# Kernel tuning notes

Hardware: AMD Instinct MI355X
Metric: run time of the kernel (lower is better)

## Reference

```python
import jax, jax.numpy as jnp
import numpy as np

# --- simulation constants (from MPMSimulator.__init__ / builder calls) ---
N_STEPS, N_SUBSTEPS = 20, 30          # 20 frames x 30 substeps = 600 iterations
G = 100                               # grid cells per axis (unit domain)
DX, INV_DX = 0.01, 100.0
DT = 5e-4                             # sim_dt
E, NU = 1.0e5, 0.3
MU = E / (2.0 * (1.0 + NU))
LAM = E * NU / ((1.0 + NU) * (1.0 - 2.0 * NU))
P_VOL = 0.005 ** 3                    # particle spacing 0.005
P_MASS = P_VOL * 3000.0               # density 3000
BOUND = 3                             # sticky boundary thickness (cells)
GRAVITY = np.array([0.0, -9.8, 0.0], np.float32)
_o = np.arange(3)
OFFS = np.stack(np.meshgrid(_o, _o, _o, indexing='ij'), -1).reshape(-1, 3).astype(np.int32)  # (27,3)


def setup_inputs() -> dict:
    key = jax.random.key(0)
    k1, k2 = jax.random.split(key)
    nx, ny, nz, sp = 30, 15, 30, 0.005   # add_mpm_grid dims, jitter=True
    gx = (np.arange(nx) - nx / 2) * sp + 0.5
    gy = np.arange(ny) * sp + 0.2
    gz = (np.arange(nz) - nz / 2) * sp + 0.5
    q = np.stack(np.meshgrid(gx, gy, gz, indexing='ij'), -1).reshape(-1, 3).astype(np.float32)
    jitter = jax.random.uniform(k1, q.shape, jnp.float32, 0.0, 0.5 * sp)
    particle_q = jnp.asarray(q) + jitter
    particle_qd = jnp.zeros_like(particle_q)
    v = jax.random.uniform(k2, (1,), jnp.float32, 0.5e-3, 1.5e-3)  # grid_m_ini value
    return {"v": v, "particle_q": particle_q, "particle_qd": particle_qd}


def _simulate(v, particle_q, particle_qd):
    vscalar = v[0]
    offs = jnp.asarray(OFFS)
    offs_f = offs.astype(jnp.float32)
    grav = jnp.asarray(GRAVITY)
    I3 = jnp.eye(3, dtype=jnp.float32)

    def substep(carry, _):
        x, vel, C, F = carry
        # update deformation gradient, neo-Hookean PK1 stress
        F = jnp.einsum('nij,njk->nik', I3 + DT * C, F)
        J = jnp.linalg.det(F)
        FinvT = jnp.swapaxes(jnp.linalg.inv(F), 1, 2)
        logJ = jnp.log(jnp.maximum(J, 1e-6))
        P = MU * (F - FinvT) + LAM * logJ[:, None, None] * FinvT
        stress = (-DT * P_VOL * 4.0 * INV_DX * INV_DX) * jnp.einsum('nij,nkj->nik', P, F)
        affine = stress + P_MASS * C

        # quadratic B-spline weights over 3x3x3 stencil
        base = jnp.floor(x * INV_DX - 0.5).astype(jnp.int32)          # (N,3)
        fx = x * INV_DX - base.astype(jnp.float32)                    # (N,3)
        w = jnp.stack([0.5 * (1.5 - fx) ** 2,
                       0.75 - (fx - 1.0) ** 2,
                       0.5 * (fx - 0.5) ** 2], 0)                     # (3,N,3)
        weight = (w[offs[:, 0], :, 0] * w[offs[:, 1], :, 1] * w[offs[:, 2], :, 2]).T  # (N,27)
        dpos = (offs_f[None] - fx[:, None, :]) * DX                   # (N,27,3)

        # P2G scatter (gravity folded into momentum, as p2g takes gravity)
        mom = weight[..., None] * (P_MASS * (vel + DT * grav)[:, None, :]
                                   + jnp.einsum('nij,nkj->nki', affine, dpos))  # (N,27,3)
        node = jnp.clip(base[:, None, :] + offs[None], 0, G - 1)
        idx = (node[..., 0] * G + node[..., 1]) * G + node[..., 2]    # (N,27)
        idxf = idx.reshape(-1)
        grid_v = jnp.zeros((G * G * G, 3), jnp.float32).at[idxf].add(mom.reshape(-1, 3))
        grid_m = jnp.zeros((G * G * G,), jnp.float32).at[idxf].add((weight * P_MASS).reshape(-1))

        # grid op: grid mass is initialized to grid_m_ini = v (set_optim_variables)
        gv = grid_v / (grid_m + vscalar)[:, None]
        gv3 = gv.reshape(G, G, G, 3)
        for axis in range(3):  # sticky-ish domain boundary (set_grid_bound)
            sh = [1, 1, 1]; sh[axis] = G
            ii = jnp.arange(G).reshape(sh)
            comp = gv3[..., axis]
            comp = jnp.where((ii < BOUND) & (comp < 0), 0.0, comp)
            comp = jnp.where((ii >= G - BOUND) & (comp > 0), 0.0, comp)
            gv3 = gv3.at[..., axis].set(comp)
        gv = gv3.reshape(-1, 3)

        # G2P gather
        gathered = gv[idx]                                            # (N,27,3)
        new_v = jnp.einsum('nk,nki->ni', weight, gathered)
        new_C = (4.0 * INV_DX * INV_DX) * jnp.einsum('nk,nki,nkj->nij', weight, gathered, dpos)
        return (x + DT * new_v, new_v, new_C, F), grid_m

    substep_ck = jax.checkpoint(substep)

    def frame(carry, _):
        carry, gms = jax.lax.scan(substep_ck, carry, None, length=N_SUBSTEPS)
        # extract_grad_tensor: grid mass of last substep (incl. grid_m_ini offset)
        return carry, gms[-1].reshape(G, G, G) + vscalar

    n = particle_q.shape[0]
    carry0 = (particle_q, particle_qd,
              jnp.zeros((n, 3, 3), jnp.float32),
              jnp.tile(I3, (n, 1, 1)))
    _, grid_m_seq = jax.lax.scan(jax.checkpoint(frame), carry0, None, length=N_STEPS)
    return grid_m_seq  # (N_STEPS, G, G, G)


def reference(v, particle_q, particle_qd):
    return _simulate(v, particle_q, particle_qd)
```

## Files before the change

kernel.cpp:

```cpp
#include <hip/hip_runtime.h>
#include <hip/hip_cooperative_groups.h>

namespace cg = cooperative_groups;

static constexpr int G    = 100;
static constexpr int G3   = G * G * G;
static constexpr int NP   = 13500;
static constexpr int NSUB = 600;
static constexpr int SPF  = 30;
static constexpr int NTHR = 512;
static constexpr int NBLK = 108;
static constexpr int TCIN  = 2048;
static constexpr int TCOUT = 2048;
static constexpr int CH   = (G3 + SPF - 2) / (SPF - 1);

__device__ __forceinline__ int clampi(int v) {
    return v < 0 ? 0 : (v > G - 1 ? G - 1 : v);
}
__device__ __forceinline__ int maxi(int a, int b) { return a > b ? a : b; }
__device__ __forceinline__ int mini(int a, int b) { return a < b ? a : b; }

__device__ __forceinline__ float4 cell_load(const float4* p) {
    const unsigned long long* q = reinterpret_cast<const unsigned long long*>(p);
    unsigned long long a = __hip_atomic_load(&q[0], __ATOMIC_RELAXED, __HIP_MEMORY_SCOPE_AGENT);
    unsigned long long b = __hip_atomic_load(&q[1], __ATOMIC_RELAXED, __HIP_MEMORY_SCOPE_AGENT);
    float4 r;
    r.x = __uint_as_float((unsigned)(a & 0xffffffffu));
    r.y = __uint_as_float((unsigned)(a >> 32));
    r.z = __uint_as_float((unsigned)(b & 0xffffffffu));
    r.w = __uint_as_float((unsigned)(b >> 32));
    return r;
}
__device__ __forceinline__ void cell_zero(float4* p) {
    unsigned long long* q = reinterpret_cast<unsigned long long*>(p);
    __hip_atomic_store(&q[0], 0ull, __ATOMIC_RELAXED, __HIP_MEMORY_SCOPE_AGENT);
    __hip_atomic_store(&q[1], 0ull, __ATOMIC_RELAXED, __HIP_MEMORY_SCOPE_AGENT);
}

__device__ __forceinline__ void gridbar(unsigned* __restrict__ cnt,
                                        unsigned* __restrict__ flag,
                                        unsigned gen) {
    __syncthreads();
    if (threadIdx.x == 0) {
        const unsigned old = __hip_atomic_fetch_add(cnt, 1u, __ATOMIC_RELAXED, __HIP_MEMORY_SCOPE_AGENT);
        if (old == gen * (unsigned)NBLK - 1u) {
            __hip_atomic_store(flag, gen, __ATOMIC_RELEASE, __HIP_MEMORY_SCOPE_AGENT);
        }
    }
    while (__hip_atomic_load(flag, __ATOMIC_RELAXED, __HIP_MEMORY_SCOPE_AGENT) < gen) { }
    asm volatile("" ::: "memory");
}

__launch_bounds__(NTHR)
__global__ void mpm_sim(const float* __restrict__ vscal,
                        const float* __restrict__ q0,
                        const float* __restrict__ qd0,
                        float* __restrict__ out,
                        float* __restrict__ ws,
                        unsigned* __restrict__ barcnt,
                        unsigned* __restrict__ barflag)
{
    const float vs = vscal[0];
    float4* const g4 = reinterpret_cast<float4*>(ws);

    cg::grid_group gg = cg::this_grid();
    const int tid = blockIdx.x * NTHR + threadIdx.x;
    const int nth = NBLK * NTHR;

    const int slot = threadIdx.x >> 2;
    const int sub  = threadIdx.x & 3;
    const bool act = slot < 125;
    int pid = 0;
    if (act) {
        const int b  = blockIdx.x;
        const int bx = b / 18;
        const int by = (b / 6) % 3;
        const int bz = b % 6;
        const int lx = slot / 25;
        const int rem = slot % 25;
        const int ly = rem / 5;
        const int lz = rem % 5;
        const int ix = bx * 5 + lx;
        const int iy = by * 5 + ly;
        const int iz = bz * 5 + lz;
        pid = (ix * 15 + iy) * 30 + iz;
    }

    const float DT      = 5e-4f;
    const float INV_DX  = 100.0f;
    const float DXc     = 0.01f;
    const float MU      = (float)(1.0e5 / (2.0 * (1.0 + 0.3)));
    const float LAM     = (float)(1.0e5 * 0.3 / ((1.0 + 0.3) * (1.0 - 0.6)));
    const float P_MASS  = (float)(0.005 * 0.005 * 0.005 * 3000.0);
    const float KS      = (float)(-5.0e-4 * (0.005 * 0.005 * 0.005) * 4.0 * 100.0 * 100.0);
    const float DTG     = (float)(5.0e-4 * (-9.8));
    const float CSC     = 4.0f * INV_DX * INV_DX;

    __shared__ float4 tileIn[TCIN];
    __shared__ float  tileOut[4 * TCOUT];
    __shared__ int sred[6];

    {
        const float4 z = make_float4(0.f, 0.f, 0.f, 0.f);
        for (int i = tid; i < 3 * G3; i += nth) g4[i] = z;
        if (tid == 0) {
            __hip_atomic_store(barcnt,  0u, __ATOMIC_RELAXED, __HIP_MEMORY_SCOPE_AGENT);
            __hip_atomic_store(barflag, 0u, __ATOMIC_RELAXED, __HIP_MEMORY_SCOPE_AGENT);
        }
    }

    float px = 0.f, py = 0.f, pz = 0.f, vx = 0.f, vy = 0.f, vz = 0.f;
    float C00 = 0.f, C01 = 0.f, C02 = 0.f,
          C10 = 0.f, C11 = 0.f, C12 = 0.f,
          C20 = 0.f, C21 = 0.f, C22 = 0.f;
    float F00 = 1.f, F01 = 0.f, F02 = 0.f,
          F10 = 0.f, F11 = 1.f, F12 = 0.f,
          F20 = 0.f, F21 = 0.f, F22 = 1.f;
    if (act) {
        px = q0[3 * pid + 0]; py = q0[3 * pid + 1]; pz = q0[3 * pid + 2];
        vx = qd0[3 * pid + 0]; vy = qd0[3 * pid + 1]; vz = qd0[3 * pid + 2];
    }

    int pmn0 = 0, pmn1 = 0, pmn2 = 0, pmx0 = -1, pmx1 = -1, pmx2 = -1; bool pvalid = false;
    int zmn0 = 0, zmn1 = 0, zmn2 = 0, zmx0 = -1, zmx1 = -1, zmx2 = -1; bool zvalid = false;

    gg.sync();

    unsigned gen = 0;

    for (int p = 0; p < NSUB; ++p) {
        const int bS = p % 3;
        const int bG = (p + 2) % 3;
        const int bZ = (p + 1) % 3;
        float4*       __restrict__ gS4 = g4 + bS * G3;
        const float4* __restrict__ gG4 = g4 + bG * G3;
        float4*       __restrict__ gZ4 = g4 + bZ * G3;
        const int fc = p % SPF;
        float* const outF = (fc == SPF - 1) ? (out + (p / SPF) * G3) : nullptr;

        const int tmn0 = pvalid ? maxi(pmn0 - 1, 0) : 0;
        const int tmn1 = pvalid ? maxi(pmn1 - 1, 0) : 0;
        const int tmn2 = pvalid ? maxi(pmn2 - 1, 0) : 0;
        const int tD0  = pvalid ? (mini(pmx0 + 1, G - 1) - tmn0 + 1) : 0;
        const int tD1  = pvalid ? (mini(pmx1 + 1, G - 1) - tmn1 + 1) : 0;
        const int tD2  = pvalid ? (mini(pmx2 + 1, G - 1) - tmn2 + 1) : 0;
        const int tvol = pvalid ? tD0 * tD1 * tD2 : 0;
        const bool fast = pvalid && (tvol <= TCOUT);

        if (threadIdx.x == 0) {
            sred[0] = INT_MAX; sred[1] = INT_MAX; sred[2] = INT_MAX;
            sred[3] = INT_MIN; sred[4] = INT_MIN; sred[5] = INT_MIN;
        }
        if (fc < SPF - 1) {
            float* of = out + (p / SPF) * G3;
            const int beg = fc * CH;
            const int end = (beg + CH < G3) ? beg + CH : G3;
            for (int i = beg + tid; i < end; i += nth)
                __hip_atomic_store(&of[i], vs, __ATOMIC_RELAXED, __HIP_MEMORY_SCOPE_AGENT);
        }
        {
            float4* t4 = reinterpret_cast<float4*>(tileOut);
            const float4 z = make_float4(0.f, 0.f, 0.f, 0.f);
            const int zn = fast ? tvol : TCOUT;
            for (int i = threadIdx.x; i < zn; i += NTHR) t4[i] = z;
        }
        if (zvalid) {
            const int zD1 = zmx1 - zmn1 + 1, zD2 = zmx2 - zmn2 + 1;
            const int zvol = (zmx0 - zmn0 + 1) * zD1 * zD2;
            for (int c = threadIdx.x; c < zvol; c += NTHR) {
                const int k = c % zD2;
                const int t = c / zD2;
                const int j = t % zD1;
                const int i = t / zD1;
                cell_zero(&gZ4[((zmn0 + i) * G + (zmn1 + j)) * G + (zmn2 + k)]);
            }
        }
        const int iD1 = pvalid ? (pmx1 - pmn1 + 1) : 0;
        const int iD2 = pvalid ? (pmx2 - pmn2 + 1) : 0;
        const int inVol = pvalid ? (pmx0 - pmn0 + 1) * iD1 * iD2 : 0;
        const bool staged = pvalid && (inVol <= TCIN);
        if (staged) {
            for (int c = threadIdx.x; c < inVol; c += NTHR) {
                const int k = c % iD2;
                const int t = c / iD2;
                const int j = t % iD1;
                const int i = t / iD1;
                const int nx = pmn0 + i, ny = pmn1 + j, nz = pmn2 + k;
                const float4 gq = cell_load(&gG4[(nx * G + ny) * G + nz]);
                const float den = gq.w + vs;
                float gvx = gq.x / den;
                float gvy = gq.y / den;
                float gvz = gq.z / den;
                if (nx < 3       && gvx < 0.f) gvx = 0.f;
                if (nx >= G - 3  && gvx > 0.f) gvx = 0.f;
                if (ny < 3       && gvy < 0.f) gvy = 0.f;
                if (ny >= G - 3  && gvy > 0.f) gvy = 0.f;
                if (nz < 3       && gvz < 0.f) gvz = 0.f;
                if (nz >= G - 3  && gvz > 0.f) gvz = 0.f;
                tileIn[c] = make_float4(gvx, gvy, gvz, 0.f);
            }
        }
        __syncthreads();

        int sb0 = 0, sb1 = 0, sb2 = 0;
        float fx0 = 0.f, fx1 = 0.f, fx2 = 0.f;
        float A00 = 0.f, A01 = 0.f, A02 = 0.f,
              A10 = 0.f, A11 = 0.f, A12 = 0.f,
              A20 = 0.f, A21 = 0.f, A22 = 0.f;
        float mvx = 0.f, mvy = 0.f, mvz = 0.f;

        if (act) {
            if (p > 0) {
                const float xs0 = px * INV_DX, xs1 = py * INV_DX, xs2 = pz * INV_DX;
                const float fb0 = floorf(xs0 - 0.5f), fb1 = floorf(xs1 - 0.5f), fb2 = floorf(xs2 - 0.5f);
                const int b0 = (int)fb0, b1 = (int)fb1, b2 = (int)fb2;
                const float gx0 = xs0 - fb0, gx1 = xs1 - fb1, gx2 = xs2 - fb2;
                float wa[3], wb[3], wc[3];
                wa[0] = 0.5f * (1.5f - gx0) * (1.5f - gx0);
                wa[1] = 0.75f - (gx0 - 1.0f) * (gx0 - 1.0f);
                wa[2] = 0.5f * (gx0 - 0.5f) * (gx0 - 0.5f);
                wb[0] = 0.5f * (1.5f - gx1) * (1.5f - gx1);
                wb[1] = 0.75f - (gx1 - 1.0f) * (gx1 - 1.0f);
                wb[2] = 0.5f * (gx1 - 0.5f) * (gx1 - 0.5f);
                wc[0] = 0.5f * (1.5f - gx2) * (1.5f - gx2);
                wc[1] = 0.75f - (gx2 - 1.0f) * (gx2 - 1.0f);
                wc[2] = 0.5f * (gx2 - 0.5f) * (gx2 - 0.5f);

                float nvx = 0.f, nvy = 0.f, nvz = 0.f;
                float nc00 = 0.f, nc01 = 0.f, nc02 = 0.f,
                      nc10 = 0.f, nc11 = 0.f, nc12 = 0.f,
                      nc20 = 0.f, nc21 = 0.f, nc22 = 0.f;
                #pragma unroll
                for (int t = 0; t < 7; ++t) {
                    const int c = sub + 4 * t;
                    if (c >= 27) break;
                    const int oi = c / 9;
                    const int rem = c - 9 * oi;
                    const int oj = rem / 3;
                    const int ok = rem - 3 * oj;
                    const int nx = clampi(b0 + oi);
                    const int ny = clampi(b1 + oj);
                    const int nz = clampi(b2 + ok);
                    const float dpx = ((float)oi - gx0) * DXc;
                    const float dpy = ((float)oj - gx1) * DXc;
                    const float dpz = ((float)ok - gx2) * DXc;
                    const float w = wa[oi] * wb[oj] * wc[ok];
                    float gvx, gvy, gvz;
                    if (staged) {
                        const float4 gv4 = tileIn[((nx - pmn0) * iD1 + (ny - pmn1)) * iD2 + (nz - pmn2)];
                        gvx = gv4.x; gvy = gv4.y; gvz = gv4.z;
                    } else {
                        const float4 gq = cell_load(&gG4[(nx * G + ny) * G + nz]);
                        const float den = gq.w + vs;
                        gvx = gq.x / den;
                        gvy = gq.y / den;
                        gvz = gq.z / den;
                        if (nx < 3       && gvx < 0.f) gvx = 0.f;
                        if (nx >= G - 3  && gvx > 0.f) gvx = 0.f;
                        if (ny < 3       && gvy < 0.f) gvy = 0.f;
                        if (ny >= G - 3  && gvy > 0.f) gvy = 0.f;
                        if (nz < 3       && gvz < 0.f) gvz = 0.f;
                        if (nz >= G - 3  && gvz > 0.f) gvz = 0.f;
                    }
                    nvx += w * gvx; nvy += w * gvy; nvz += w * gvz;
                    const float wgx = w * gvx, wgy = w * gvy, wgz = w * gvz;
                    nc00 += wgx * dpx; nc01 += wgx * dpy; nc02 += wgx * dpz;
                    nc10 += wgy * dpx; nc11 += wgy * dpy; nc12 += wgy * dpz;
                    nc20 += wgz * dpx; nc21 += wgz * dpy; nc22 += wgz * dpz;
                }
                #define BFLY(v) { v += __shfl_xor(v, 1); v += __shfl_xor(v, 2); }
                BFLY(nvx) BFLY(nvy) BFLY(nvz)
                BFLY(nc00) BFLY(nc01) BFLY(nc02)
                BFLY(nc10) BFLY(nc11) BFLY(nc12)
                BFLY(nc20) BFLY(nc21) BFLY(nc22)
                #undef BFLY
                vx = nvx; vy = nvy; vz = nvz;
                C00 = CSC * nc00; C01 = CSC * nc01; C02 = CSC * nc02;
                C10 = CSC * nc10; C11 = CSC * nc11; C12 = CSC * nc12;
                C20 = CSC * nc20; C21 = CSC * nc21; C22 = CSC * nc22;
                px += DT * vx; py += DT * vy; pz += DT * vz;
            }

            {
                const float t00 = F00 + DT * (C00 * F00 + C01 * F10 + C02 * F20);
                const float t01 = F01 + DT * (C00 * F01 + C01 * F11 + C02 * F21);
                const float t02 = F02 + DT * (C00 * F02 + C01 * F12 + C02 * F22);
                const float t10 = F10 + DT * (C10 * F00 + C11 * F10 + C12 * F20);
                const float t11 = F11 + DT * (C10 * F01 + C11 * F11 + C12 * F21);
                const float t12 = F12 + DT * (C10 * F02 + C11 * F12 + C12 * F22);
                const float t20 = F20 + DT * (C20 * F00 + C21 * F10 + C22 * F20);
                const float t21 = F21 + DT * (C20 * F01 + C21 * F11 + C22 * F21);
                const float t22 = F22 + DT * (C20 * F02 + C21 * F12 + C22 * F22);
                F00 = t00; F01 = t01; F02 = t02;
                F10 = t10; F11 = t11; F12 = t12;
                F20 = t20; F21 = t21; F22 = t22;
            }

            const float c00 = F11 * F22 - F12 * F21;
            const float c01 = F12 * F20 - F10 * F22;
            const float c02 = F10 * F21 - F11 * F20;
            const float det = F00 * c00 + F01 * c01 + F02 * c02;
            const float c10 = F02 * F21 - F01 * F22;
            const float c11 = F00 * F22 - F02 * F20;
            const float c12 = F01 * F20 - F00 * F21;
            const float c20 = F01 * F12 - F02 * F11;
            const float c21 = F02 * F10 - F00 * F12;
            const float c22 = F00 * F11 - F01 * F10;
            const float idet = 1.0f / det;
            const float lj = LAM * logf(fmaxf(det, 1e-6f));
            const float fit00 = c00 * idet, fit01 = c01 * idet, fit02 = c02 * idet;
            const float fit10 = c10 * idet, fit11 = c11 * idet, fit12 = c12 * idet;
            const float fit20 = c20 * idet, fit21 = c21 * idet, fit22 = c22 * idet;
            const float P00 = MU * (F00 - fit00) + lj * fit00;
            const float P01 = MU * (F01 - fit01) + lj * fit01;
            const float P02 = MU * (F02 - fit02) + lj * fit02;
            const float P10 = MU * (F10 - fit10) + lj * fit10;
            const float P11 = MU * (F11 - fit11) + lj * fit11;
            const float P12 = MU * (F12 - fit12) + lj * fit12;
            const float P20 = MU * (F20 - fit20) + lj * fit20;
            const float P21 = MU * (F21 - fit21) + lj * fit21;
            const float P22 = MU * (F22 - fit22) + lj * fit22;
            A00 = KS * (P00 * F00 + P01 * F01 + P02 * F02) + P_MASS * C00;
            A01 = KS * (P00 * F10 + P01 * F11 + P02 * F12) + P_MASS * C01;
            A02 = KS * (P00 * F20 + P01 * F21 + P02 * F22) + P_MASS * C02;
            A10 = KS * (P10 * F00 + P11 * F01 + P12 * F02) + P_MASS * C10;
            A11 = KS * (P10 * F10 + P11 * F11 + P12 * F12) + P_MASS * C11;
            A12 = KS * (P10 * F20 + P11 * F21 + P12 * F22) + P_MASS * C12;
            A20 = KS * (P20 * F00 + P21 * F01 + P22 * F02) + P_MASS * C20;
            A21 = KS * (P20 * F10 + P21 * F11 + P22 * F12) + P_MASS * C21;
            A22 = KS * (P20 * F20 + P21 * F21 + P22 * F22) + P_MASS * C22;

            const float xs0 = px * INV_DX, xs1 = py * INV_DX, xs2 = pz * INV_DX;
            const float fb0 = floorf(xs0 - 0.5f), fb1 = floorf(xs1 - 0.5f), fb2 = floorf(xs2 - 0.5f);
            sb0 = (int)fb0; sb1 = (int)fb1; sb2 = (int)fb2;
            fx0 = xs0 - fb0; fx1 = xs1 - fb1; fx2 = xs2 - fb2;
            mvx = P_MASS * vx;
            mvy = P_MASS * (vy + DTG);
            mvz = P_MASS * vz;

            if (sub == 0) {
                atomicMin(&sred[0], clampi(sb0)); atomicMax(&sred[3], clampi(sb0 + 2));
                atomicMin(&sred[1], clampi(sb1)); atomicMax(&sred[4], clampi(sb1 + 2));
                atomicMin(&sred[2], clampi(sb2)); atomicMax(&sred[5], clampi(sb2 + 2));
            }
        }

        float wa0 = 0.f, wa1 = 0.f, wa2 = 0.f, wb0 = 0.f, wb1 = 0.f, wb2 = 0.f,
              wcc0 = 0.f, wcc1 = 0.f, wcc2 = 0.f;
        if (act) {
            wa0 = 0.5f * (1.5f - fx0) * (1.5f - fx0);
            wa1 = 0.75f - (fx0 - 1.0f) * (fx0 - 1.0f);
            wa2 = 0.5f * (fx0 - 0.5f) * (fx0 - 0.5f);
            wb0 = 0.5f * (1.5f - fx1) * (1.5f - fx1);
            wb1 = 0.75f - (fx1 - 1.0f) * (fx1 - 1.0f);
            wb2 = 0.5f * (fx1 - 0.5f) * (fx1 - 0.5f);
            wcc0 = 0.5f * (1.5f - fx2) * (1.5f - fx2);
            wcc1 = 0.75f - (fx2 - 1.0f) * (fx2 - 1.0f);
            wcc2 = 0.5f * (fx2 - 0.5f) * (fx2 - 0.5f);
        }
        const float WA[3] = { wa0, wa1, wa2 };
        const float WB[3] = { wb0, wb1, wb2 };
        const float WC[3] = { wcc0, wcc1, wcc2 };

        if (fast) {
            if (act) {
                #pragma unroll
                for (int t = 0; t < 7; ++t) {
                    const int c = sub + 4 * t;
                    if (c >= 27) break;
                    const int oi = c / 9;
                    const int rem = c - 9 * oi;
                    const int oj = rem / 3;
                    const int ok = rem - 3 * oj;
                    const int li  = clampi(sb0 + oi) - tmn0;
                    const int lj2 = clampi(sb1 + oj) - tmn1;
                    const int lk  = clampi(sb2 + ok) - tmn2;
                    const float dpx = ((float)oi - fx0) * DXc;
                    const float dpy = ((float)oj - fx1) * DXc;
                    const float dpz = ((float)ok - fx2) * DXc;
                    const float w = WA[oi] * WB[oj] * WC[ok];
                    const int c4 = 4 * ((li * tD1 + lj2) * tD2 + lk);
                    atomicAdd(&tileOut[c4 + 0], w * (mvx + A00 * dpx + A01 * dpy + A02 * dpz));
                    atomicAdd(&tileOut[c4 + 1], w * (mvy + A10 * dpx + A11 * dpy + A12 * dpz));
                    atomicAdd(&tileOut[c4 + 2], w * (mvz + A20 * dpx + A21 * dpy + A22 * dpz));
                    atomicAdd(&tileOut[c4 + 3], w * P_MASS);
                }
            }
            __syncthreads();
            for (int c = threadIdx.x; c < tvol; c += NTHR) {
                const float m = tileOut[4 * c + 3];
                if (m != 0.f) {
                    const int k = c % tD2;
                    const int t = c / tD2;
                    const int j = t % tD1;
                    const int i = t / tD1;
                    const int gidx = ((tmn0 + i) * G + (tmn1 + j)) * G + (tmn2 + k);
                    float* gp = reinterpret_cast<float*>(gS4 + gidx);
                    unsafeAtomicAdd(gp + 0, tileOut[4 * c + 0]);
                    unsafeAtomicAdd(gp + 1, tileOut[4 * c + 1]);
                    unsafeAtomicAdd(gp + 2, tileOut[4 * c + 2]);
                    unsafeAtomicAdd(gp + 3, m);
                    if (outF) unsafeAtomicAdd(&outF[gidx], m);
                }
            }
        } else {
            __syncthreads();
            const int mn0 = sred[0], mn1 = sred[1], mn2 = sred[2];
            const int mx0 = sred[3], mx1 = sred[4], mx2 = sred[5];
            const bool anyAct = (mx0 >= mn0);
            const int D1 = mx1 - mn1 + 1, D2 = mx2 - mn2 + 1;
            const int vol = anyAct ? (mx0 - mn0 + 1) * D1 * D2 : 0;
            const bool useLDS = anyAct && (vol <= TCOUT);
            if (useLDS) {
                if (act) {
                    #pragma unroll
                    for (int t = 0; t < 7; ++t) {
                        const int c = sub + 4 * t;
                        if (c >= 27) break;
                        const int oi = c / 9;
                        const int rem = c - 9 * oi;
                        const int oj = rem / 3;
                        const int ok = rem - 3 * oj;
                        const int li  = clampi(sb0 + oi) - mn0;
                        const int lj2 = clampi(sb1 + oj) - mn1;
                        const int lk  = clampi(sb2 + ok) - mn2;
                        const float dpx = ((float)oi - fx0) * DXc;
                        const float dpy = ((float)oj - fx1) * DXc;
                        const float dpz = ((float)ok - fx2) * DXc;
                        const float w = WA[oi] * WB[oj] * WC[ok];
                        const int c4 = 4 * ((li * D1 + lj2) * D2 + lk);
                        atomicAdd(&tileOut[c4 + 0], w * (mvx + A00 * dpx + A01 * dpy + A02 * dpz));
                        atomicAdd(&tileOut[c4 + 1], w * (mvy + A10 * dpx + A11 * dpy + A12 * dpz));
                        atomicAdd(&tileOut[c4 + 2], w * (mvz + A20 * dpx + A21 * dpy + A22 * dpz));
                        atomicAdd(&tileOut[c4 + 3], w * P_MASS);
                    }
                }
                __syncthreads();
                for (int c = threadIdx.x; c < vol; c += NTHR) {
                    const float m = tileOut[4 * c + 3];
                    if (m != 0.f) {
                        const int k = c % D2;
                        const int t = c / D2;
                        const int j = t % D1;
                        const int i = t / D1;
                        const int gidx = ((mn0 + i) * G + (mn1 + j)) * G + (mn2 + k);
                        float* gp = reinterpret_cast<float*>(gS4 + gidx);
                        unsafeAtomicAdd(gp + 0, tileOut[4 * c + 0]);
                        unsafeAtomicAdd(gp + 1, tileOut[4 * c + 1]);
                        unsafeAtomicAdd(gp + 2, tileOut[4 * c + 2]);
                        unsafeAtomicAdd(gp + 3, m);
                        if (outF) unsafeAtomicAdd(&outF[gidx], m);
                    }
                }
            } else {
                if (anyAct && act) {
                    #pragma unroll
                    for (int t = 0; t < 7; ++t) {
                        const int c = sub + 4 * t;
                        if (c >= 27) break;
                        const int oi = c / 9;
                        const int rem = c - 9 * oi;
                        const int oj = rem / 3;
                        const int ok = rem - 3 * oj;
                        const int nx = clampi(sb0 + oi);
                        const int ny = clampi(sb1 + oj);
                        const int nz = clampi(sb2 + ok);
                        const float dpx = ((float)oi - fx0) * DXc;
                        const float dpy = ((float)oj - fx1) * DXc;
                        const float dpz = ((float)ok - fx2) * DXc;
                        const float w = WA[oi] * WB[oj] * WC[ok];
                        const int gidx = (nx * G + ny) * G + nz;
                        float* gp = reinterpret_cast<float*>(gS4 + gidx);
                        unsafeAtomicAdd(gp + 0, w * (mvx + A00 * dpx + A01 * dpy + A02 * dpz));
                        unsafeAtomicAdd(gp + 1, w * (mvy + A10 * dpx + A11 * dpy + A12 * dpz));
                        unsafeAtomicAdd(gp + 2, w * (mvz + A20 * dpx + A21 * dpy + A22 * dpz));
                        unsafeAtomicAdd(gp + 3, w * P_MASS);
                        if (outF) unsafeAtomicAdd(&outF[gidx], w * P_MASS);
                    }
                }
                __syncthreads();
            }
        }

        zmn0 = pmn0; zmn1 = pmn1; zmn2 = pmn2;
        zmx0 = pmx0; zmx1 = pmx1; zmx2 = pmx2; zvalid = pvalid;
        pmn0 = sred[0]; pmn1 = sred[1]; pmn2 = sred[2];
        pmx0 = sred[3]; pmx1 = sred[4]; pmx2 = sred[5]; pvalid = (pmx0 >= pmn0);

        if (p < NSUB - 1) gridbar(barcnt, barflag, ++gen);
    }
}

extern "C" void kernel_launch(void* const* d_in, const int* in_sizes, int n_in,
                              void* d_out, int out_size, void* d_ws, size_t ws_size,
                              hipStream_t stream) {
    const float* v  = (const float*)d_in[0];
    const float* q  = (const float*)d_in[1];
    const float* qd = (const float*)d_in[2];
    float* out = (float*)d_out;
    float* ws  = (float*)d_ws;
    char* tail = (char*)d_ws + (ws_size & ~(size_t)255);
    unsigned* barcnt  = reinterpret_cast<unsigned*>(tail - 256);
    unsigned* barflag = reinterpret_cast<unsigned*>(tail - 512);
    void* args[] = { (void*)&v, (void*)&q, (void*)&qd, (void*)&out, (void*)&ws,
                     (void*)&barcnt, (void*)&barflag };
    hipLaunchCooperativeKernel(reinterpret_cast<void*>(mpm_sim),
                               dim3(NBLK), dim3(NTHR), args, 0, stream);
}
```

Measured before the change: 17.49 ms.

## Use LDS-only barriers and single-thread global spin in grid barrier

Replaces __syncthreads with a custom barrier that waits only on LDS counters (lgkmcnt) instead of all outstanding memory ops. The grid barrier now has only thread 0 spin on the global flag and broadcast via a shared-memory flag, so the other threads stop polling global memory. Zeroing and output-fill work is moved after the staged input load so global stores can stay in flight across the block barrier. This risks memory-ordering bugs, because the global stores and atomics are no longer drained before barriers.

Measured after the change: 17.28 ms. About the same (-1.2%).

```diff
diff --git a/kernel.cpp b/kernel.cpp
--- a/kernel.cpp
+++ b/kernel.cpp
@@ -1,5 +1,6 @@
 #include <hip/hip_runtime.h>
 #include <hip/hip_cooperative_groups.h>
+#include <climits>
 
 namespace cg = cooperative_groups;
 
@@ -37,18 +38,11 @@
     __hip_atomic_store(&q[1], 0ull, __ATOMIC_RELAXED, __HIP_MEMORY_SCOPE_AGENT);
 }
 
-__device__ __forceinline__ void gridbar(unsigned* __restrict__ cnt,
-                                        unsigned* __restrict__ flag,
-                                        unsigned gen) {
-    __syncthreads();
-    if (threadIdx.x == 0) {
-        const unsigned old = __hip_atomic_fetch_add(cnt, 1u, __ATOMIC_RELAXED, __HIP_MEMORY_SCOPE_AGENT);
-        if (old == gen * (unsigned)NBLK - 1u) {
-            __hip_atomic_store(flag, gen, __ATOMIC_RELEASE, __HIP_MEMORY_SCOPE_AGENT);
-        }
-    }
-    while (__hip_atomic_load(flag, __ATOMIC_RELAXED, __HIP_MEMORY_SCOPE_AGENT) < gen) { }
-    asm volatile("" ::: "memory");
+__device__ __forceinline__ void bar_lds() {
+    __builtin_amdgcn_sched_barrier(0);
+    asm volatile("s_waitcnt lgkmcnt(0)" ::: "memory");
+    __builtin_amdgcn_s_barrier();
+    __builtin_amdgcn_sched_barrier(0);
 }
 
 __launch_bounds__(NTHR)
@@ -99,6 +93,7 @@
     __shared__ float4 tileIn[TCIN];
     __shared__ float  tileOut[4 * TCOUT];
     __shared__ int sred[6];
+    __shared__ unsigned lflag;
 
     {
         const float4 z = make_float4(0.f, 0.f, 0.f, 0.f);
@@ -107,6 +102,7 @@
             __hip_atomic_store(barcnt,  0u, __ATOMIC_RELAXED, __HIP_MEMORY_SCOPE_AGENT);
             __hip_atomic_store(barflag, 0u, __ATOMIC_RELAXED, __HIP_MEMORY_SCOPE_AGENT);
         }
+        if (threadIdx.x == 0) lflag = 0u;
     }
 
     float px = 0.f, py = 0.f, pz = 0.f, vx = 0.f, vy = 0.f, vz = 0.f;
@@ -147,34 +143,6 @@
         const int tvol = pvalid ? tD0 * tD1 * tD2 : 0;
         const bool fast = pvalid && (tvol <= TCOUT);
 
-        if (threadIdx.x == 0) {
-            sred[0] = INT_MAX; sred[1] = INT_MAX; sred[2] = INT_MAX;
-            sred[3] = INT_MIN; sred[4] = INT_MIN; sred[5] = INT_MIN;
-        }
-        if (fc < SPF - 1) {
-            float* of = out + (p / SPF) * G3;
-            const int beg = fc * CH;
-            const int end = (beg + CH < G3) ? beg + CH : G3;
-            for (int i = beg + tid; i < end; i += nth)
-                __hip_atomic_store(&of[i], vs, __ATOMIC_RELAXED, __HIP_MEMORY_SCOPE_AGENT);
-        }
-        {
-            float4* t4 = reinterpret_cast<float4*>(tileOut);
-            const float4 z = make_float4(0.f, 0.f, 0.f, 0.f);
-            const int zn = fast ? tvol : TCOUT;
-            for (int i = threadIdx.x; i < zn; i += NTHR) t4[i] = z;
-        }
-        if (zvalid) {
-            const int zD1 = zmx1 - zmn1 + 1, zD2 = zmx2 - zmn2 + 1;
-            const int zvol = (zmx0 - zmn0 + 1) * zD1 * zD2;
-            for (int c = threadIdx.x; c < zvol; c += NTHR) {
-                const int k = c % zD2;
-                const int t = c / zD2;
-                const int j = t % zD1;
-                const int i = t / zD1;
-                cell_zero(&gZ4[((zmn0 + i) * G + (zmn1 + j)) * G + (zmn2 + k)]);
-            }
-        }
         const int iD1 = pvalid ? (pmx1 - pmn1 + 1) : 0;
         const int iD2 = pvalid ? (pmx2 - pmn2 + 1) : 0;
         const int inVol = pvalid ? (pmx0 - pmn0 + 1) * iD1 * iD2 : 0;
@@ -200,7 +168,35 @@
                 tileIn[c] = make_float4(gvx, gvy, gvz, 0.f);
             }
         }
-        __syncthreads();
+        {
+            float4* t4 = reinterpret_cast<float4*>(tileOut);
+            const float4 z = make_float4(0.f, 0.f, 0.f, 0.f);
+            const int zn = fast ? tvol : TCOUT;
+            for (int i = threadIdx.x; i < zn; i += NTHR) t4[i] = z;
+        }
+        if (zvalid) {
+            const int zD1 = zmx1 - zmn1 + 1, zD2 = zmx2 - zmn2 + 1;
+            const int zvol = (zmx0 - zmn0 + 1) * zD1 * zD2;
+            for (int c = threadIdx.x; c < zvol; c += NTHR) {
+                const int k = c % zD2;
+                const int t = c / zD2;
+                const int j = t % zD1;
+                const int i = t / zD1;
+                cell_zero(&gZ4[((zmn0 + i) * G + (zmn1 + j)) * G + (zmn2 + k)]);
+            }
+        }
+        if (fc < SPF - 1) {
+            float* of = out + (p / SPF) * G3;
+            const int beg = fc * CH;
+            const int end = (beg + CH < G3) ? beg + CH : G3;
+            for (int i = beg + tid; i < end; i += nth)
+                __hip_atomic_store(&of[i], vs, __ATOMIC_RELAXED, __HIP_MEMORY_SCOPE_AGENT);
+        }
+        if (threadIdx.x == 0) {
+            sred[0] = INT_MAX; sred[1] = INT_MAX; sred[2] = INT_MAX;
+            sred[3] = INT_MIN; sred[4] = INT_MIN; sred[5] = INT_MIN;
+        }
+        bar_lds();
 
         int sb0 = 0, sb1 = 0, sb2 = 0;
         float fx0 = 0.f, fx1 = 0.f, fx2 = 0.f;
@@ -386,7 +382,7 @@
                     atomicAdd(&tileOut[c4 + 3], w * P_MASS);
                 }
             }
-            __syncthreads();
+            bar_lds();
             for (int c = threadIdx.x; c < tvol; c += NTHR) {
                 const float m = tileOut[4 * c + 3];
                 if (m != 0.f) {
@@ -404,7 +400,7 @@
                 }
             }
         } else {
-            __syncthreads();
+            bar_lds();
             const int mn0 = sred[0], mn1 = sred[1], mn2 = sred[2];
             const int mx0 = sred[3], mx1 = sred[4], mx2 = sred[5];
             const bool anyAct = (mx0 >= mn0);
@@ -435,7 +431,7 @@
                         atomicAdd(&tileOut[c4 + 3], w * P_MASS);
                     }
                 }
-                __syncthreads();
+                bar_lds();
                 for (int c = threadIdx.x; c < vol; c += NTHR) {
                     const float m = tileOut[4 * c + 3];
                     if (m != 0.f) {
@@ -478,7 +474,7 @@
                         if (outF) unsafeAtomicAdd(&outF[gidx], w * P_MASS);
                     }
                 }
-                __syncthreads();
+                bar_lds();
             }
         }
 
@@ -487,7 +483,20 @@
         pmn0 = sred[0]; pmn1 = sred[1]; pmn2 = sred[2];
         pmx0 = sred[3]; pmx1 = sred[4]; pmx2 = sred[5]; pvalid = (pmx0 >= pmn0);
 
-        if (p < NSUB - 1) gridbar(barcnt, barflag, ++gen);
+        if (p < NSUB - 1) {
+            ++gen;
+            __syncthreads();
+            if (threadIdx.x == 0) {
+                const unsigned old = __hip_atomic_fetch_add(barcnt, 1u, __ATOMIC_RELAXED, __HIP_MEMORY_SCOPE_AGENT);
+                if (old == gen * (unsigned)NBLK - 1u) {
+                    __hip_atomic_store(barflag, gen, __ATOMIC_RELEASE, __HIP_MEMORY_SCOPE_AGENT);
+                }
+                while (__hip_atomic_load(barflag, __ATOMIC_RELAXED, __HIP_MEMORY_SCOPE_AGENT) < gen) { }
+                __hip_atomic_store(&lflag, gen, __ATOMIC_RELAXED, __HIP_MEMORY_SCOPE_WORKGROUP);
+            }
+            while (__hip_atomic_load(&lflag, __ATOMIC_RELAXED, __HIP_MEMORY_SCOPE_WORKGROUP) < gen) { }
+            asm volatile("" ::: "memory");
+        }
     }
 }
 
```
